# Kernel optimization log

Measured on AMD Instinct MI355X. Metric: run time of the kernel, lower is better.

## Reference

```python
import jax, jax.numpy as jnp
import numpy as np

B, N, C = 16, 2048, 3           # images, proposals/image, classes (incl. background)
K = 100                         # num_detections kept per class
SCORE_THRESH = 0.05
NMS_THRESH = 0.5
MIN_ANGLE = 10.0                # process_box min width (self.min_angle)
WX, WW = 1.0, 1.0               # box_coder reg_weights
NEG = jnp.float32(-1e9)


def setup_inputs() -> dict:
    key = jax.random.key(0)
    k1, k2, k3, k4 = jax.random.split(key, 4)
    class_logit = jax.random.normal(k1, (B, N, C), jnp.float32)
    box_regression = jax.random.normal(k2, (B, N, 2 * C), jnp.float32) * 0.1
    starts = jax.random.uniform(k3, (B, N), dtype=jnp.float32) * 300.0
    widths = jax.random.uniform(k4, (B, N), dtype=jnp.float32) * 50.0 + 12.0
    proposal = jnp.stack([starts, starts + widths], axis=-1)  # [B,N,2] 1-D intervals
    return {"class_logit": class_logit, "box_regression": box_regression,
            "proposal": proposal, "image_shape": 360}


def _decode(delta, prop):
    w = prop[:, 1] - prop[:, 0]
    ctr = prop[:, 0] + 0.5 * w
    dx = delta[:, 0] / WX
    dw = jnp.minimum(delta[:, 1] / WW, 4.0)  # clamp like torchvision
    pc = dx * w + ctr
    pw = jnp.exp(dw) * w
    return jnp.stack([pc - 0.5 * pw, pc + 0.5 * pw], axis=-1)  # [N,2]


def _iou_1d(a, b):
    inter = jnp.maximum(0.0, jnp.minimum(a[:, None, 1], b[None, :, 1])
                        - jnp.maximum(a[:, None, 0], b[None, :, 0]))
    union = (a[:, None, 1] - a[:, None, 0]) + (b[None, :, 1] - b[None, :, 0]) - inter
    return inter / jnp.maximum(union, 1e-8)  # [Na,Nb]


def _infer_one_class(score, delta, prop, image_shape):
    # score [N], delta [N,2], prop [N,2] -> [K,3] (start, end, score); invalid slots score=NEG
    box = _decode(delta, prop)
    lo = jnp.clip(box[:, 0], 0.0, image_shape)
    hi = jnp.clip(box[:, 1], 0.0, image_shape)
    box = jnp.stack([lo, hi], axis=-1)
    valid = ((hi - lo) >= MIN_ANGLE) & (score >= SCORE_THRESH)
    ms = jnp.where(valid, score, NEG)
    order = jnp.argsort(-ms)
    b = box[order]
    s = ms[order]
    sup = jax.lax.stop_gradient(_iou_1d(b, b)) > NMS_THRESH  # [N,N] bool
    idx = jnp.arange(N)

    def body(keep, i):  # greedy NMS in score order
        kill = sup[i] & keep[i] & (idx > i)
        return keep & ~kill, None

    keep0 = s > 0.5 * NEG
    keep, _ = jax.lax.scan(body, keep0, idx)
    ks = jnp.where(keep, s, NEG)
    top_s, top_i = jax.lax.top_k(ks, K)
    top_b = b[top_i]
    return jnp.concatenate([top_b, top_s[:, None]], axis=-1)  # [K,3]


def reference(class_logit, box_regression, proposal, image_shape):
    img = jnp.float32(image_shape)
    scores = jax.nn.softmax(class_logit, axis=-1)[..., 1:]        # [B,N,C-1] fg classes
    deltas = box_regression.reshape(B, N, C, 2)[:, :, 1:]         # [B,N,C-1,2]
    scores = jnp.moveaxis(scores, -1, 1)                          # [B,C-1,N]
    deltas = jnp.moveaxis(deltas, 2, 1)                           # [B,C-1,N,2]
    f = jax.vmap(jax.vmap(_infer_one_class, in_axes=(0, 0, None, None)),
                 in_axes=(0, 0, 0, None))
    return f(scores, deltas, proposal, img)  # [B, C-1, K, 3]
```

## Files before the change

kernel.cpp:

```cpp
#include <hip/hip_runtime.h>
#include <math.h>

#define B_IMG 16
#define N_PROP 2048
#define C_CLS 3
#define K_OUT 100
#define NTHREADS 1024
#define NWAVES (NTHREADS / 64)
#define NBLK64 (N_PROP / 64)

__device__ __forceinline__ unsigned long long shfl_xor_u64(unsigned long long v, int lx) {
    unsigned int lo = (unsigned int)__shfl_xor((int)(unsigned int)(v & 0xffffffffull), lx, 64);
    unsigned int hi = (unsigned int)__shfl_xor((int)(unsigned int)(v >> 32), lx, 64);
    return ((unsigned long long)hi << 32) | (unsigned long long)lo;
}
__device__ __forceinline__ float readlane_f(float v, int l) {
    return __int_as_float(__builtin_amdgcn_readlane(__float_as_int(v), l));
}
__device__ __forceinline__ bool iou_gt_half(float inter, float uni) {
    double b = (double)fmaxf(uni, 1e-8f);
    return (double)inter * 2.0 > b * 0x1.000001p0;
}

__global__ __launch_bounds__(NTHREADS)
void roiheads_kernel(const float* __restrict__ class_logit,
                     const float* __restrict__ box_reg,
                     const float* __restrict__ proposal,
                     const int* __restrict__ image_shape_p,
                     float* __restrict__ out)
{
#pragma clang fp contract(off)
    __shared__ unsigned long long skey[N_PROP];
    __shared__ float llo[N_PROP], lhi[N_PROP];
    __shared__ float slo[N_PROP], shi[N_PROP];
    __shared__ unsigned char keep[N_PROP];
    __shared__ unsigned short alv[2][N_PROP];
    __shared__ float clo[64], chi[64];
    __shared__ unsigned long long kmask[NBLK64];
    __shared__ int wsum[NWAVES];
    __shared__ int sh_nvalid, sh_ccnt;

    const int tid = threadIdx.x;
    const int lane = tid & 63;
    const int wid = tid >> 6;
    const int img = blockIdx.x >> 1;
    const int cls = blockIdx.x & 1;

    int raw = image_shape_p[0];
    float imgf = (raw > 0 && raw < 1000000) ? (float)raw : __int_as_float(raw);

    if (tid == 0) sh_nvalid = 0;

    const int p0 = (wid << 7) | (lane << 1);
    const int p1 = p0 | 1;

    auto decode = [&](int n) -> unsigned long long {
#pragma clang fp contract(off)
        const float* lg = class_logit + ((size_t)img * N_PROP + n) * C_CLS;
        float l0 = lg[0], l1 = lg[1], l2 = lg[2];
        float mx = fmaxf(l0, fmaxf(l1, l2));
        float e0 = (float)exp((double)(l0 - mx));
        float e1 = (float)exp((double)(l1 - mx));
        float e2 = (float)exp((double)(l2 - mx));
        float denom = (e0 + e1) + e2;
        float ec = (cls == 0) ? e1 : e2;
        float score = ec / denom;

        const float* dr = box_reg + ((size_t)img * N_PROP + n) * (2 * C_CLS) + 2 * (cls + 1);
        float dx = dr[0];
        float dw = fminf(dr[1], 4.0f);
        const float* pp = proposal + ((size_t)img * N_PROP + n) * 2;
        float pA = pp[0], pB = pp[1];
        float w = pB - pA;
        float ctr = pA + 0.5f * w;
        float t = dx * w;
        float pc = t + ctr;
        float pw = (float)exp((double)dw) * w;
        float half = 0.5f * pw;
        float lo = pc - half;
        float hi = pc + half;
        lo = fminf(fmaxf(lo, 0.0f), imgf);
        hi = fminf(fmaxf(hi, 0.0f), imgf);
        bool valid = ((hi - lo) >= 10.0f) && (score >= 0.05f);
        float ms = valid ? score : -1e9f;

        llo[n] = lo; lhi[n] = hi;
        unsigned int u = __float_as_uint(ms);
        unsigned int e = (u & 0x80000000u) ? ~u : (u | 0x80000000u);
        return ((unsigned long long)e << 32) |
               (unsigned long long)(0xFFFFFFFFu - (unsigned int)n);
    };
    unsigned long long r0 = decode(p0);
    unsigned long long r1 = decode(p1);

    auto pass_inreg = [&](int k, int j) {
        if (j == 1) {
            bool desc = ((p0 & k) == 0);
            bool sw = desc ? (r0 < r1) : (r0 > r1);
            if (sw) { unsigned long long t = r0; r0 = r1; r1 = t; }
        } else {
            int lx = j >> 1;
            unsigned long long o0 = shfl_xor_u64(r0, lx);
            unsigned long long o1 = shfl_xor_u64(r1, lx);
            bool desc = ((p0 & k) == 0);
            bool lower = ((p0 & j) == 0);
            bool takeMax = (lower == desc);
            r0 = takeMax ? (r0 > o0 ? r0 : o0) : (r0 < o0 ? r0 : o0);
            r1 = takeMax ? (r1 > o1 ? r1 : o1) : (r1 < o1 ? r1 : o1);
        }
    };

    for (int k = 2; k <= 128; k <<= 1)
        for (int j = k >> 1; j >= 1; j >>= 1)
            pass_inreg(k, j);

    for (int k = 256; k <= N_PROP; k <<= 1) {
        skey[p0] = r0; skey[p1] = r1;
        __syncthreads();
        for (int j = k >> 1; j >= 128; j >>= 1) {
            int i = ((tid & ~(j - 1)) << 1) | (tid & (j - 1));
            int part = i | j;
            unsigned long long a = skey[i], b = skey[part];
            bool desc_blk = ((i & k) == 0);
            bool sw = desc_blk ? (a < b) : (a > b);
            if (sw) { skey[i] = b; skey[part] = a; }
            __syncthreads();
        }
        r0 = skey[p0]; r1 = skey[p1];
        for (int j = 64; j >= 1; j >>= 1)
            pass_inreg(k, j);
    }
    skey[p0] = r0; skey[p1] = r1;
    __syncthreads();

    for (int i = tid; i < N_PROP; i += NTHREADS) {
        unsigned long long kk = skey[i];
        unsigned int e = (unsigned int)(kk >> 32);
        unsigned int sb = (e & 0x80000000u) ? (e & 0x7FFFFFFFu) : ~e;
        float s = __uint_as_float(sb);
        unsigned int n = 0xFFFFFFFFu - (unsigned int)(kk & 0xFFFFFFFFull);
        slo[i] = llo[n];
        shi[i] = lhi[n];
        keep[i] = 0;
        bool v = (s > -5e8f);
        unsigned long long mb = __ballot(v);
        if (lane == 0) atomicAdd(&sh_nvalid, __popcll(mb));
        alv[0][i] = (unsigned short)i;
    }
    __syncthreads();

    int na = sh_nvalid;
    int cur = 0;
    const unsigned long long below = (1ull << lane) - 1ull;

    while (na > 0) {
        const int m = (na < 64) ? na : 64;
        if (tid < 64) {
            bool inr = (lane < m);
            unsigned short p = inr ? alv[cur][lane] : (unsigned short)0;
            float blo = inr ? slo[p] : 0.0f;
            float bhi = inr ? shi[p] : 0.0f;
            float bw = bhi - blo;
            unsigned long long A = (m >= 64) ? ~0ull : ((1ull << m) - 1ull);
            unsigned long long kept = 0;
            while (A) {
                int c = __builtin_ctzll(A);
                float cl = readlane_f(blo, c);
                float ch = readlane_f(bhi, c);
                float inter = fmaxf(fminf(bhi, ch) - fmaxf(blo, cl), 0.0f);
                float uni = bw + (ch - cl) - inter;
                bool kill = (lane > c) && iou_gt_half(inter, uni);
                unsigned long long row = __ballot(kill);
                kept |= (1ull << c);
                A &= ~(row | (1ull << c));
            }
            bool alive = inr && ((kept >> lane) & 1ull);
            if (alive) keep[p] = 1;
            int rank = __popcll(kept & below);
            if (alive) { clo[rank] = blo; chi[rank] = bhi; }
            if (lane == 0) sh_ccnt = __popcll(kept);
        }
        __syncthreads();
        const int cnt = sh_ccnt;

        float klo = 0.0f, khi = 0.0f;
        if (lane < cnt) { klo = clo[lane]; khi = chi[lane]; }
        int base = 0;
        for (int start = 64; start < na; start += NTHREADS) {
            int t = start + tid;
            unsigned short q = 0;
            bool surv = false;
            if (t < na) {
                q = alv[cur][t];
                float qlo = slo[q], qhi = shi[q];
                float qw = qhi - qlo;
                bool dead = false;
                for (int r = 0; r < cnt; ++r) {
                    float cl = readlane_f(klo, r);
                    float ch = readlane_f(khi, r);
                    float inter = fmaxf(fminf(qhi, ch) - fmaxf(qlo, cl), 0.0f);
                    float uni = qw + (ch - cl) - inter;
                    dead |= iou_gt_half(inter, uni);
                }
                surv = !dead;
            }
            unsigned long long mb = __ballot(surv);
            if (lane == 0) wsum[wid] = __popcll(mb);
            __syncthreads();
            int off = base, tot = base;
            for (int w2 = 0; w2 < NWAVES; ++w2) {
                int c2 = wsum[w2];
                if (w2 < wid) off += c2;
                tot += c2;
            }
            if (surv) alv[cur ^ 1][off + __popcll(mb & below)] = q;
            base = tot;
            __syncthreads();
        }
        na = base;
        cur ^= 1;
    }

    for (int blk = wid; blk < NBLK64; blk += NWAVES) {
        bool kk = keep[blk * 64 + lane] != 0;
        unsigned long long mb = __ballot(kk);
        if (lane == 0) kmask[blk] = mb;
    }
    __syncthreads();
    {
        float* outp = out + (((size_t)img * 2 + cls) * K_OUT) * 3;
        for (int blk = wid; blk < NBLK64; blk += NWAVES) {
            int kc = 0, nc = 0, nk = 0;
            for (int b = 0; b < NBLK64; ++b) {
                int pc = __popcll(kmask[b]);
                nk += pc;
                if (b < blk) { kc += pc; nc += 64 - pc; }
            }
            if (kc >= K_OUT && nk + nc >= K_OUT && nc >= K_OUT) continue;
            int p = blk * 64 + lane;
            unsigned long long mb = kmask[blk];
            bool k = (mb >> lane) & 1ull;
            int rk = kc + __popcll(mb & below);
            int rn = nc + __popcll((~mb) & below);
            if (k) {
                if (rk < K_OUT) {
                    unsigned long long kk2 = skey[p];
                    unsigned int e = (unsigned int)(kk2 >> 32);
                    unsigned int sb = (e & 0x80000000u) ? (e & 0x7FFFFFFFu) : ~e;
                    outp[rk * 3 + 0] = slo[p];
                    outp[rk * 3 + 1] = shi[p];
                    outp[rk * 3 + 2] = __uint_as_float(sb);
                }
            } else {
                int oi = nk + rn;
                if (oi < K_OUT) {
                    outp[oi * 3 + 0] = slo[p];
                    outp[oi * 3 + 1] = shi[p];
                    outp[oi * 3 + 2] = -1e9f;
                }
            }
        }
    }
}

extern "C" void kernel_launch(void* const* d_in, const int* in_sizes, int n_in,
                              void* d_out, int out_size, void* d_ws, size_t ws_size,
                              hipStream_t stream) {
    const float* class_logit = (const float*)d_in[0];
    const float* box_reg     = (const float*)d_in[1];
    const float* prop        = (const float*)d_in[2];
    const int*   image_shape = (const int*)d_in[3];
    float* out = (float*)d_out;

    roiheads_kernel<<<dim3(B_IMG * 2), dim3(NTHREADS), 0, stream>>>(
        class_logit, box_reg, prop, image_shape, out);
}
```

Baseline: 98.51 us.

## Build 128-candidate NMS suppression matrix in parallel across all waves

Each NMS round now takes a 128-box head instead of 64. All 16 waves compute the pairwise IoU suppression bitmasks for that head into shared memory, replacing the serial single-wave loop that computed IoU per chosen pivot. Every wave then resolves the greedy keep set redundantly from those bitmasks using readlane. The larger head is meant to halve the number of rounds and barriers. In exchange it adds extra IoU work and two-part loops when pruning the remaining candidates.

```diff
diff --git a/kernel.cpp b/kernel.cpp
--- a/kernel.cpp
+++ b/kernel.cpp
@@ -16,6 +16,11 @@
 }
 __device__ __forceinline__ float readlane_f(float v, int l) {
     return __int_as_float(__builtin_amdgcn_readlane(__float_as_int(v), l));
+}
+__device__ __forceinline__ unsigned long long readlane_u64(unsigned long long v, int l) {
+    unsigned int lo = (unsigned int)__builtin_amdgcn_readlane((int)(unsigned int)(v & 0xffffffffull), l);
+    unsigned int hi = (unsigned int)__builtin_amdgcn_readlane((int)(unsigned int)(v >> 32), l);
+    return ((unsigned long long)hi << 32) | (unsigned long long)lo;
 }
 __device__ __forceinline__ bool iou_gt_half(float inter, float uni) {
     double b = (double)fmaxf(uni, 1e-8f);
@@ -35,10 +40,11 @@
     __shared__ float slo[N_PROP], shi[N_PROP];
     __shared__ unsigned char keep[N_PROP];
     __shared__ unsigned short alv[2][N_PROP];
-    __shared__ float clo[64], chi[64];
+    __shared__ unsigned long long sup0[128], sup1[128];
+    __shared__ float clo[128], chi[128];
     __shared__ unsigned long long kmask[NBLK64];
     __shared__ int wsum[NWAVES];
-    __shared__ int sh_nvalid, sh_ccnt;
+    __shared__ int sh_nvalid;
 
     const int tid = threadIdx.x;
     const int lane = tid & 63;
@@ -154,39 +160,65 @@
     const unsigned long long below = (1ull << lane) - 1ull;
 
     while (na > 0) {
-        const int m = (na < 64) ? na : 64;
-        if (tid < 64) {
-            bool inr = (lane < m);
-            unsigned short p = inr ? alv[cur][lane] : (unsigned short)0;
-            float blo = inr ? slo[p] : 0.0f;
-            float bhi = inr ? shi[p] : 0.0f;
-            float bw = bhi - blo;
-            unsigned long long A = (m >= 64) ? ~0ull : ((1ull << m) - 1ull);
-            unsigned long long kept = 0;
-            while (A) {
-                int c = __builtin_ctzll(A);
-                float cl = readlane_f(blo, c);
-                float ch = readlane_f(bhi, c);
-                float inter = fmaxf(fminf(bhi, ch) - fmaxf(blo, cl), 0.0f);
-                float uni = bw + (ch - cl) - inter;
-                bool kill = (lane > c) && iou_gt_half(inter, uni);
-                unsigned long long row = __ballot(kill);
-                kept |= (1ull << c);
-                A &= ~(row | (1ull << c));
-            }
-            bool alive = inr && ((kept >> lane) & 1ull);
-            if (alive) keep[p] = 1;
-            int rank = __popcll(kept & below);
-            if (alive) { clo[rank] = blo; chi[rank] = bhi; }
-            if (lane == 0) sh_ccnt = __popcll(kept);
+        const int m = (na < 128) ? na : 128;
+
+        for (int i = 0; i < 16; ++i) {
+            int u = (wid << 4) | i;
+            int rr = u >> 1, h = u & 1;
+            unsigned long long mb = 0;
+            if (!(h == 0 && rr >= 64)) {
+                unsigned short pr = alv[cur][rr];
+                float rlo = slo[pr], rhi = shi[pr];
+                int jc = (h << 6) | lane;
+                unsigned short pq = alv[cur][jc];
+                float qlo = slo[pq], qhi = shi[pq];
+                float inter = fmaxf(fminf(rhi, qhi) - fmaxf(rlo, qlo), 0.0f);
+                float uni = ((rhi - rlo) + (qhi - qlo)) - inter;
+                bool kill = (jc > rr) && iou_gt_half(inter, uni);
+                mb = __ballot(kill);
+            }
+            if (lane == 0) { if (h == 0) sup0[rr] = mb; else sup1[rr] = mb; }
         }
         __syncthreads();
-        const int cnt = sh_ccnt;
-
-        float klo = 0.0f, khi = 0.0f;
-        if (lane < cnt) { klo = clo[lane]; khi = chi[lane]; }
+
+        unsigned long long rw00 = sup0[lane];
+        unsigned long long rw01 = sup1[lane];
+        unsigned long long rw11 = sup1[64 + lane];
+        unsigned long long A0 = (m >= 64) ? ~0ull : ((1ull << m) - 1ull);
+        unsigned long long A1 = (m > 64) ? ((m >= 128) ? ~0ull : ((1ull << (m - 64)) - 1ull)) : 0ull;
+        unsigned long long k0 = 0, k1 = 0;
+        while (A0) {
+            int c = __builtin_ctzll(A0);
+            k0 |= (1ull << c);
+            A0 &= ~(readlane_u64(rw00, c) | (1ull << c));
+            A1 &= ~readlane_u64(rw01, c);
+        }
+        while (A1) {
+            int c = __builtin_ctzll(A1);
+            k1 |= (1ull << c);
+            A1 &= ~(readlane_u64(rw11, c) | (1ull << c));
+        }
+        const int cnt0 = __popcll(k0);
+        const int cnt = cnt0 + __popcll(k1);
+
+        if (tid < 128) {
+            unsigned long long km = (tid < 64) ? k0 : k1;
+            bool alive = (tid < m) && ((km >> lane) & 1ull);
+            if (alive) {
+                unsigned short p = alv[cur][tid];
+                keep[p] = 1;
+                int rank = __popcll(km & below) + ((tid < 64) ? 0 : cnt0);
+                clo[rank] = slo[p]; chi[rank] = shi[p];
+            }
+        }
+        __syncthreads();
+
+        float klo0 = 0.0f, khi0 = 0.0f, klo1 = 0.0f, khi1 = 0.0f;
+        if (lane < cnt) { klo0 = clo[lane]; khi0 = chi[lane]; }
+        if (64 + lane < cnt) { klo1 = clo[64 + lane]; khi1 = chi[64 + lane]; }
+        const int c1 = (cnt < 64) ? cnt : 64;
         int base = 0;
-        for (int start = 64; start < na; start += NTHREADS) {
+        for (int start = m; start < na; start += NTHREADS) {
             int t = start + tid;
             unsigned short q = 0;
             bool surv = false;
@@ -195,11 +227,18 @@
                 float qlo = slo[q], qhi = shi[q];
                 float qw = qhi - qlo;
                 bool dead = false;
-                for (int r = 0; r < cnt; ++r) {
-                    float cl = readlane_f(klo, r);
-                    float ch = readlane_f(khi, r);
+                for (int r = 0; r < c1; ++r) {
+                    float cl = readlane_f(klo0, r);
+                    float ch = readlane_f(khi0, r);
                     float inter = fmaxf(fminf(qhi, ch) - fmaxf(qlo, cl), 0.0f);
-                    float uni = qw + (ch - cl) - inter;
+                    float uni = (qw + (ch - cl)) - inter;
+                    dead |= iou_gt_half(inter, uni);
+                }
+                for (int r = 64; r < cnt; ++r) {
+                    float cl = readlane_f(klo1, r - 64);
+                    float ch = readlane_f(khi1, r - 64);
+                    float inter = fmaxf(fminf(qhi, ch) - fmaxf(qlo, cl), 0.0f);
+                    float uni = (qw + (ch - cl)) - inter;
                     dead |= iou_gt_half(inter, uni);
                 }
                 surv = !dead;
```

Result: slower. 106.7 us (+8.4%).
